# Kernel tuning notes

Hardware: AMD Instinct MI355X
Metric: run time of the kernel (lower is better)

The kernel has to match this reference:

```python
import jax, jax.numpy as jnp
import numpy as np

P, Q, R = 6, 0, 0
N = P + Q + R
DIM = 1 << N  # 64 basis blades


def _cayley_table(p, q, r):
    """Dense [dim, dim, dim] Cayley tensor C with C[a, b, a^b] = sign(a, b).
    Basis blades are indexed by bitmasks; sign combines the canonical
    reordering parity with the metric signature (+1 x p, -1 x q, 0 x r)."""
    n = p + q + r
    dim = 1 << n
    metric = [1.0] * p + [-1.0] * q + [0.0] * r
    C = np.zeros((dim, dim, dim), dtype=np.float32)
    for a in range(dim):
        for b in range(dim):
            # reorder parity: count transpositions to sort blade product
            s = 1.0
            aa = a >> 1
            cnt = 0
            while aa:
                cnt += bin(aa & b).count('1')
                aa >>= 1
            if cnt & 1:
                s = -s
            # metric contribution from repeated basis vectors
            for i in range(n):
                if (a >> i) & 1 and (b >> i) & 1:
                    s *= metric[i]
            C[a, b, a ^ b] = s
    return C

CAYLEY = jnp.asarray(_cayley_table(P, Q, R))  # [64, 64, 64], highly sparse


def setup_inputs() -> dict:
    key = jax.random.key(0)
    kx, kw = jax.random.split(key)
    x = jax.random.normal(kx, (1048576, DIM), dtype=jnp.float32)
    weight = jax.random.normal(kw, (DIM,), dtype=jnp.float32)
    return {"x": x, "weight": weight}


def reference(x, weight):
    # geometric_product(x, weight) with weight broadcast over the batch:
    # out[b, k] = sum_{i,j} C[i, j, k] * x[b, i] * weight[j]
    # Contract C with the shared weight first (tiny [dim, dim] matrix),
    # then apply to every batch element.
    M = jnp.einsum('ijk,j->ik', CAYLEY, weight)  # [64, 64]
    return x @ M  # [B, 64]
```

## Files before the change

kernel.cpp:

```cpp
#include <hip/hip_runtime.h>
#include <hip/hip_bf16.h>


#define DIM 64
#define TPB 256
#define ROWS 64

typedef __attribute__((ext_vector_type(8))) short  bf16x8;
typedef __attribute__((ext_vector_type(4))) float  f32x4;

typedef const unsigned int __attribute__((address_space(1)))* gu32p;
typedef unsigned int __attribute__((address_space(3)))* su32p;

__device__ __forceinline__ unsigned short f2bf(float v) {
    __hip_bfloat16 hb = __float2bfloat16(v);
    return *reinterpret_cast<unsigned short*>(&hb);
}

__global__ void build_Mt(const float* __restrict__ w, unsigned short* __restrict__ Mt) {
    int t = threadIdx.x + blockIdx.x * blockDim.x;
    if (t >= 8 * 64 * 8) return;
    int f  = t >> 9;
    int kc = f >> 2, ab = f & 3;
    int rem = t & 511;
    int l = rem >> 3, e = rem & 7;
    int k = kc * 32 + ((l >> 4) << 3) + e;
    int a = (ab << 4) + (l & 15);
    int j = k ^ a;
    int aa = k >> 1, cnt = 0;
    while (aa) { cnt += __popc(aa & j); aa >>= 1; }
    float v = (cnt & 1) ? -w[j] : w[j];
    Mt[t] = f2bf(v);
}

__global__ __launch_bounds__(TPB, 8)
void gp_main_kernel(const float* __restrict__ x,
                    const unsigned short* __restrict__ Mt,
                    float* __restrict__ out) {
    __shared__ float xs[ROWS * DIM];

    const int tid  = threadIdx.x;
    const int lane = tid & 63;
    const int wv   = tid >> 6;
    const int r15  = lane & 15;
    const int g    = lane >> 4;

    const long long rowbase = (long long)blockIdx.x * ROWS;
    const float4* __restrict__ xin = (const float4*)x;

    #pragma unroll
    for (int it = 0; it < 4; ++it) {
        int idx  = it * TPB + tid;
        int row  = idx >> 4;
        int f4   = idx & 15;
        int c    = ((f4 >> 1) ^ (row & 7));
        long long src = (rowbase + row) * 16 + c * 2 + (f4 & 1);
        __builtin_amdgcn_global_load_lds((gu32p)(xin + src),
                                         (su32p)&xs[idx * 4], 16, 0, 0);
    }

    bf16x8 af[2][4];
    const bf16x8* __restrict__ Mtv = (const bf16x8*)Mt;
    #pragma unroll
    for (int kc = 0; kc < 2; ++kc)
        #pragma unroll
        for (int ab = 0; ab < 4; ++ab)
            af[kc][ab] = Mtv[(kc * 4 + ab) * 64 + lane];

    __syncthreads();

    const int r_loc = wv * 16 + r15;
    bf16x8 bfr[2];
    #pragma unroll
    for (int kc = 0; kc < 2; ++kc) {
        int s = (kc * 4 + g) ^ (r_loc & 7);
        const float* src = &xs[r_loc * DIM + s * 8];
        float4 lo = *reinterpret_cast<const float4*>(src);
        float4 hi = *reinterpret_cast<const float4*>(src + 4);
        bf16x8 t;
        t[0] = (short)f2bf(lo.x); t[1] = (short)f2bf(lo.y);
        t[2] = (short)f2bf(lo.z); t[3] = (short)f2bf(lo.w);
        t[4] = (short)f2bf(hi.x); t[5] = (short)f2bf(hi.y);
        t[6] = (short)f2bf(hi.z); t[7] = (short)f2bf(hi.w);
        bfr[kc] = t;
    }

    f32x4 acc[4];
    #pragma unroll
    for (int ab = 0; ab < 4; ++ab) acc[ab] = (f32x4){0.f, 0.f, 0.f, 0.f};
    #pragma unroll
    for (int kc = 0; kc < 2; ++kc)
        #pragma unroll
        for (int ab = 0; ab < 4; ++ab)
            acc[ab] = __builtin_amdgcn_mfma_f32_16x16x32_bf16(
                af[kc][ab], bfr[kc], acc[ab], 0, 0, 0);

    float4* __restrict__ outp = (float4*)out;
    const long long rg = rowbase + r_loc;
    #pragma unroll
    for (int ab = 0; ab < 4; ++ab)
        outp[rg * 16 + ab * 4 + g] =
            make_float4(acc[ab][0], acc[ab][1], acc[ab][2], acc[ab][3]);
}

extern "C" void kernel_launch(void* const* d_in, const int* in_sizes, int n_in,
                              void* d_out, int out_size, void* d_ws, size_t ws_size,
                              hipStream_t stream) {
    const float* x = (const float*)d_in[0];
    const float* w = (const float*)d_in[1];
    float* out = (float*)d_out;
    unsigned short* Mt = (unsigned short*)d_ws;

    int nrows = in_sizes[0] / DIM;
    int nblocks = nrows / ROWS;

    build_Mt<<<16, 256, 0, stream>>>(w, Mt);
    gp_main_kernel<<<nblocks, TPB, 0, stream>>>(x, Mt, out);
}
```

Measured before the change: 103.0 us.

## Make blocks persistent over eight tiles with double-buffered LDS prefetch

Each block now processes eight 64-row tiles instead of one. Tile loads go through two LDS buffers, with the next tile prefetched by global_load_lds while the current one is converted and multiplied, and hand-placed vmcnt waits and barriers keep the buffers ordered. The aim is to overlap memory latency with compute and to spread the per-block Mt fragment loads over more rows. The cost is double the shared memory per block, a lower launch-bounds occupancy target (5 instead of 8), and one eighth as many blocks.

```diff
diff --git a/kernel.cpp b/kernel.cpp
--- a/kernel.cpp
+++ b/kernel.cpp
@@ -5,6 +5,7 @@
 #define DIM 64
 #define TPB 256
 #define ROWS 64
+#define NT   8
 
 typedef __attribute__((ext_vector_type(8))) short  bf16x8;
 typedef __attribute__((ext_vector_type(4))) float  f32x4;
@@ -33,11 +34,11 @@
     Mt[t] = f2bf(v);
 }
 
-__global__ __launch_bounds__(TPB, 8)
+__global__ __launch_bounds__(TPB, 5)
 void gp_main_kernel(const float* __restrict__ x,
                     const unsigned short* __restrict__ Mt,
                     float* __restrict__ out) {
-    __shared__ float xs[ROWS * DIM];
+    __shared__ float xs[2][ROWS * DIM];
 
     const int tid  = threadIdx.x;
     const int lane = tid & 63;
@@ -45,19 +46,9 @@
     const int r15  = lane & 15;
     const int g    = lane >> 4;
 
-    const long long rowbase = (long long)blockIdx.x * ROWS;
+    const long long tile0 = (long long)blockIdx.x * NT;
     const float4* __restrict__ xin = (const float4*)x;
-
-    #pragma unroll
-    for (int it = 0; it < 4; ++it) {
-        int idx  = it * TPB + tid;
-        int row  = idx >> 4;
-        int f4   = idx & 15;
-        int c    = ((f4 >> 1) ^ (row & 7));
-        long long src = (rowbase + row) * 16 + c * 2 + (f4 & 1);
-        __builtin_amdgcn_global_load_lds((gu32p)(xin + src),
-                                         (su32p)&xs[idx * 4], 16, 0, 0);
-    }
+    float4* __restrict__ outp = (float4*)out;
 
     bf16x8 af[2][4];
     const bf16x8* __restrict__ Mtv = (const bf16x8*)Mt;
@@ -67,40 +58,66 @@
         for (int ab = 0; ab < 4; ++ab)
             af[kc][ab] = Mtv[(kc * 4 + ab) * 64 + lane];
 
-    __syncthreads();
+    auto STAGE = [&](int t, int buf) {
+        #pragma unroll
+        for (int it = 0; it < 4; ++it) {
+            int idx  = it * TPB + tid;
+            int row  = idx >> 4;
+            int f4   = idx & 15;
+            int c    = ((f4 >> 1) ^ (row & 7));
+            long long src = ((tile0 + t) * ROWS + row) * 16 + c * 2 + (f4 & 1);
+            __builtin_amdgcn_global_load_lds((gu32p)(xin + src),
+                                             (su32p)&xs[buf][idx * 4], 16, 0, 0);
+        }
+    };
 
-    const int r_loc = wv * 16 + r15;
-    bf16x8 bfr[2];
+    STAGE(0, 0);
+    STAGE(1, 1);
+
     #pragma unroll
-    for (int kc = 0; kc < 2; ++kc) {
-        int s = (kc * 4 + g) ^ (r_loc & 7);
-        const float* src = &xs[r_loc * DIM + s * 8];
-        float4 lo = *reinterpret_cast<const float4*>(src);
-        float4 hi = *reinterpret_cast<const float4*>(src + 4);
-        bf16x8 t;
-        t[0] = (short)f2bf(lo.x); t[1] = (short)f2bf(lo.y);
-        t[2] = (short)f2bf(lo.z); t[3] = (short)f2bf(lo.w);
-        t[4] = (short)f2bf(hi.x); t[5] = (short)f2bf(hi.y);
-        t[6] = (short)f2bf(hi.z); t[7] = (short)f2bf(hi.w);
-        bfr[kc] = t;
-    }
+    for (int t = 0; t < NT; ++t) {
+        const int cur = t & 1;
+        if (t == 0 || t == NT - 1) asm volatile("s_waitcnt vmcnt(4)" ::: "memory");
+        else                       asm volatile("s_waitcnt vmcnt(8)" ::: "memory");
+        __builtin_amdgcn_s_barrier();
+        __builtin_amdgcn_sched_barrier(0);
 
-    f32x4 acc[4];
-    #pragma unroll
-    for (int ab = 0; ab < 4; ++ab) acc[ab] = (f32x4){0.f, 0.f, 0.f, 0.f};
-    #pragma unroll
-    for (int kc = 0; kc < 2; ++kc)
+        const int r_loc = wv * 16 + r15;
+        bf16x8 bfr[2];
+        #pragma unroll
+        for (int kc = 0; kc < 2; ++kc) {
+            int s = (kc * 4 + g) ^ (r_loc & 7);
+            const float* src = &xs[cur][r_loc * DIM + s * 8];
+            float4 lo = *reinterpret_cast<const float4*>(src);
+            float4 hi = *reinterpret_cast<const float4*>(src + 4);
+            bf16x8 tt;
+            tt[0] = (short)f2bf(lo.x); tt[1] = (short)f2bf(lo.y);
+            tt[2] = (short)f2bf(lo.z); tt[3] = (short)f2bf(lo.w);
+            tt[4] = (short)f2bf(hi.x); tt[5] = (short)f2bf(hi.y);
+            tt[6] = (short)f2bf(hi.z); tt[7] = (short)f2bf(hi.w);
+            bfr[kc] = tt;
+        }
+
+        f32x4 acc[4];
+        #pragma unroll
+        for (int ab = 0; ab < 4; ++ab) acc[ab] = (f32x4){0.f, 0.f, 0.f, 0.f};
+        #pragma unroll
+        for (int kc = 0; kc < 2; ++kc)
+            #pragma unroll
+            for (int ab = 0; ab < 4; ++ab)
+                acc[ab] = __builtin_amdgcn_mfma_f32_16x16x32_bf16(
+                    af[kc][ab], bfr[kc], acc[ab], 0, 0, 0);
+
+        const long long rg = (tile0 + t) * ROWS + r_loc;
         #pragma unroll
         for (int ab = 0; ab < 4; ++ab)
-            acc[ab] = __builtin_amdgcn_mfma_f32_16x16x32_bf16(
-                af[kc][ab], bfr[kc], acc[ab], 0, 0, 0);
+            outp[rg * 16 + ab * 4 + g] =
+                make_float4(acc[ab][0], acc[ab][1], acc[ab][2], acc[ab][3]);
 
-    float4* __restrict__ outp = (float4*)out;
-    const long long rg = rowbase + r_loc;
-    #pragma unroll
-    for (int ab = 0; ab < 4; ++ab)
-        outp[rg * 16 + ab * 4 + g] =
-            make_float4(acc[ab][0], acc[ab][1], acc[ab][2], acc[ab][3]);
+        __builtin_amdgcn_s_barrier();
+        __builtin_amdgcn_sched_barrier(0);
+        if (t + 2 < NT) STAGE(t + 2, cur);
+    }
 }
 
 extern "C" void kernel_launch(void* const* d_in, const int* in_sizes, int n_in,
@@ -112,7 +129,7 @@
     unsigned short* Mt = (unsigned short*)d_ws;
 
     int nrows = in_sizes[0] / DIM;
-    int nblocks = nrows / ROWS;
+    int nblocks = nrows / (ROWS * NT);
 
     build_Mt<<<16, 256, 0, stream>>>(w, Mt);
     gp_main_kernel<<<nblocks, TPB, 0, stream>>>(x, Mt, out);
```

Result: slower. 115.3 us (+12.0%).
